# Performance work log

Measured on AMD Instinct MI355X. Metric: run time of the kernel, lower is better.

Reference implementation:

```python
import jax, jax.numpy as jnp
import numpy as np
from jax import lax
import math

B, CH, BINS, CROP = 8, 2, 1024, 1024
NUM_BANDS = 4
FF = 2048
EPS = 1e-5
SCALE = 0.02  # weight init scale for numeric stability


def _inorm(x, g, b):
    # InstanceNorm2d: x [B, C, H, W], normalize over (H, W) per (B, C); biased var
    m = x.mean(axis=(2, 3), keepdims=True)
    v = x.var(axis=(2, 3), keepdims=True)
    return (x - m) / jnp.sqrt(v + EPS) * g[None, :, None, None] + b[None, :, None, None]


def _dwconv(x, k):
    # depthwise conv1d: x [B, bins, W], k [bins, 1, 3], padding=1, groups=bins
    return lax.conv_general_dilated(x, k, (1,), [(1, 1)],
                                    dimension_numbers=('NCH', 'OIH', 'NCH'),
                                    feature_group_count=x.shape[1])


def setup_inputs() -> dict:
    key = jax.random.key(0)
    ks = jax.random.split(key, 12)
    inp = {
        'x': jax.random.normal(ks[0], (B, CH, BINS, CROP), jnp.float32),
        'prev_qk': jax.random.normal(ks[1], (B, NUM_BANDS, CROP, CROP), jnp.float32),
        'g_in': jnp.ones((CROP,), jnp.float32),
        'b_in': jnp.zeros((CROP,), jnp.float32),
        'W_in': jax.random.normal(ks[2], (1, CH), jnp.float32) * SCALE,
        'bias_in': jnp.zeros((1,), jnp.float32),
        'g1': jnp.ones((CROP,), jnp.float32),
        'b1': jnp.zeros((CROP,), jnp.float32),
        'Wq': jax.random.normal(ks[3], (BINS, BINS), jnp.float32) * SCALE,
        'Wk': jax.random.normal(ks[4], (BINS, BINS), jnp.float32) * SCALE,
        'Wv': jax.random.normal(ks[5], (BINS, BINS), jnp.float32) * SCALE,
        'Wo': jax.random.normal(ks[6], (BINS, BINS), jnp.float32) * SCALE,
        'kq': jax.random.normal(ks[7], (BINS, 1, 3), jnp.float32) * SCALE,
        'kk': jax.random.normal(ks[8], (BINS, 1, 3), jnp.float32) * SCALE,
        'kv': jax.random.normal(ks[9], (BINS, 1, 3), jnp.float32) * SCALE,
        'pos_w': jax.random.normal(ks[10], (BINS // NUM_BANDS, CROP), jnp.float32) * SCALE,
        'g2': jnp.ones((CROP,), jnp.float32),
        'b2': jnp.zeros((CROP,), jnp.float32),
        'W_ff': jax.random.normal(ks[11], (1, 2), jnp.float32) * SCALE,
        'bias_ff': jnp.zeros((1,), jnp.float32),
        'W1': jax.random.normal(jax.random.fold_in(key, 100), (FF, BINS), jnp.float32) * SCALE,
        'W2': jax.random.normal(jax.random.fold_in(key, 101), (BINS, FF), jnp.float32) * SCALE,
    }
    return inp


def reference(x, prev_qk, g_in, b_in, W_in, bias_in, g1, b1, Wq, Wk, Wv, Wo,
              kq, kk, kv, pos_w, g2, b2, W_ff, bias_ff, W1, W2):
    b = x.shape[0]
    nb = NUM_BANDS
    hd = BINS // nb
    # in_norm + in_project: transposed layout [B, CROP, BINS, CH]
    xt = jnp.transpose(x, (0, 3, 2, 1))
    xt = _inorm(xt, g_in, b_in)
    xt = jnp.einsum('bwhc,oc->bwho', xt, W_in) + bias_in  # [B,CROP,BINS,1]
    x0 = jnp.transpose(xt, (0, 3, 2, 1))                  # [B,1,BINS,CROP]
    # norm1 + attention over frames (w == CROP, c == BINS)
    h = jnp.transpose(_inorm(jnp.transpose(x0, (0, 3, 2, 1)), g1, b1), (0, 3, 2, 1))
    a_in = jnp.transpose(h, (0, 3, 2, 1))[..., 0]         # [B, W, BINS]
    q = jnp.einsum('bwc,oc->bwo', a_in, Wq)
    q = jnp.transpose(_dwconv(jnp.transpose(q, (0, 2, 1)), kq), (0, 2, 1))
    k = jnp.einsum('bwc,oc->bwo', a_in, Wk)
    k = jnp.transpose(_dwconv(jnp.transpose(k, (0, 2, 1)), kk), (0, 2, 1))
    v = jnp.einsum('bwc,oc->bwo', a_in, Wv)
    v = jnp.transpose(_dwconv(jnp.transpose(v, (0, 2, 1)), kv), (0, 2, 1))
    q4 = jnp.transpose(q.reshape(b, CROP, nb, hd), (0, 2, 1, 3))   # [B,nb,W,hd]
    k4 = jnp.transpose(k.reshape(b, CROP, nb, hd), (0, 2, 3, 1))   # [B,nb,hd,W]
    v4 = jnp.transpose(v.reshape(b, CROP, nb, hd), (0, 2, 1, 3))   # [B,nb,W,hd]
    # relative-position bias via pad-and-shift
    p = jnp.matmul(q4, pos_w)                                      # [B,nb,W,CROP]
    p = jnp.pad(p, ((0, 0), (0, 0), (0, 0), (1, 0)))
    p = jnp.swapaxes(p, 2, 3)[:, :, 1:, :]                         # [B,nb,CROP,W]
    qk = (jnp.matmul(q4, k4) + p) / math.sqrt(BINS)
    qk = qk + prev_qk
    a = jax.nn.softmax(qk, axis=-1)
    o = jnp.transpose(jnp.matmul(a, v4), (0, 2, 1, 3)).reshape(b, CROP, BINS)
    o = jnp.einsum('bwc,oc->bwo', o, Wo)                           # [B,W,BINS]
    h4 = jnp.transpose(o[..., None], (0, 3, 2, 1))                 # [B,1,BINS,CROP]
    x1 = jnp.concatenate([x0, h4], axis=1)                         # [B,2,BINS,CROP]
    # norm2 + ff_project + squared-ReLU FFN
    hn = _inorm(jnp.transpose(x1, (0, 3, 2, 1)), g2, b2)           # [B,CROP,BINS,2]
    hn = jnp.einsum('bwhc,oc->bwho', hn, W_ff) + bias_ff           # [B,CROP,BINS,1]
    hn = jnp.transpose(hn, (0, 3, 2, 1))                           # [B,1,BINS,CROP]
    ht = jnp.swapaxes(hn, 2, 3)                                    # [B,1,CROP,BINS]
    ht = jnp.square(jax.nn.relu(jnp.einsum('bowc,fc->bowf', ht, W1)))
    ht = jnp.einsum('bowf,cf->bowc', ht, W2)
    hf = jnp.swapaxes(ht, 2, 3)                                    # [B,1,BINS,CROP]
    out = jnp.concatenate([x1, hf], axis=1)                        # [B,3,BINS,CROP]
    return out, qk
```

## Files before the change

### kernel.cpp

```cpp
#include <hip/hip_runtime.h>
#include <stdint.h>

#define DEVI __device__ __forceinline__

typedef __attribute__((ext_vector_type(8))) short bf16x8;
typedef __attribute__((ext_vector_type(4))) float f32x4;

#define B_    8
#define CROP_ 1024
#define BINS_ 1024
#define NB_   4
#define HD_   256
#define FF_   2048
#define EPSF  1e-5f
#define OUT0_ELEMS (8ull*3ull*1024ull*1024ull)
#define MBYTE (1024ull*1024ull)
#define M1ELEM (1024ll*1024ll)
#define SMCAP 8.0f

DEVI unsigned short f2bf(float f) {
  unsigned u = __builtin_bit_cast(unsigned, f);
  u += 0x7fffu + ((u >> 16) & 1u);
  return (unsigned short)(u >> 16);
}
DEVI float bf2f(unsigned short h) {
  unsigned u = ((unsigned)h) << 16;
  return __builtin_bit_cast(float, u);
}

DEVI void gload16(const unsigned short* g, unsigned short* l) {
  __builtin_amdgcn_global_load_lds(
      (const __attribute__((address_space(1))) unsigned int*)g,
      (__attribute__((address_space(3))) unsigned int*)l, 16, 0, 0);
}

DEVI void xcdswz(int& bx, int& by, int& bz) {
  int gx = gridDim.x, gy = gridDim.y;
  int nwg = gx*gy*gridDim.z;
  int flat = blockIdx.x + gx*(blockIdx.y + gy*blockIdx.z);
  int s = (flat & 7)*(nwg >> 3) + (flat >> 3);
  bx = s % gx; s /= gx;
  by = s % gy;
  bz = s / gy;
}

__global__ __launch_bounds__(256) void k_conv_all(
    const float* __restrict__ Wq, const float* __restrict__ Wk,
    const float* __restrict__ Wv, const float* __restrict__ Wo,
    const float* __restrict__ W1, const float* __restrict__ W2,
    const float* __restrict__ pw,
    unsigned short* __restrict__ WQKVB, unsigned short* __restrict__ WOB,
    unsigned short* __restrict__ W1B, unsigned short* __restrict__ W2B,
    unsigned short* __restrict__ PWT) {
  long long i = (long long)blockIdx.x*256 + threadIdx.x;
  long long stride = (long long)gridDim.x*256;
  const long long total = 8*M1ELEM + (1 << 18);
  for (; i < total; i += stride) {
    if (i < 3*M1ELEM) {
      const float* s = i < M1ELEM ? Wq : (i < 2*M1ELEM ? Wk : Wv);
      WQKVB[i] = f2bf(s[i & (M1ELEM-1)]);
    } else if (i < 4*M1ELEM) { WOB[i-3*M1ELEM] = f2bf(Wo[i-3*M1ELEM]); }
    else if (i < 6*M1ELEM)   { W1B[i-4*M1ELEM] = f2bf(W1[i-4*M1ELEM]); }
    else if (i < 8*M1ELEM)   { W2B[i-6*M1ELEM] = f2bf(W2[i-6*M1ELEM]); }
    else {
      long long j = i - 8*M1ELEM;
      int w = (int)(j >> 8), d = (int)(j & 255);
      PWT[j] = f2bf(pw[d*1024 + w]);
    }
  }
}

__global__ __launch_bounds__(256) void k_instx0(const float* __restrict__ x,
    const float* __restrict__ g_in, const float* __restrict__ b_in,
    const float* __restrict__ W_in, const float* __restrict__ bias_in,
    float* __restrict__ outp, float* __restrict__ x0t) {
  int b = blockIdx.y, w0 = blockIdx.x*32;
  int t = threadIdx.x, wl = t & 31, p = t >> 5;
  const float* xb = x + (size_t)b*2*M1ELEM + w0 + wl;
  float s = 0.f, ss = 0.f;
  for (int i = p*256; i < p*256 + 256; ++i) {
    float v = xb[(size_t)i*CROP_];
    s += v; ss += v*v;
  }
  __shared__ float ls[8][32], lss[8][32];
  __shared__ float s_coef[32], s_add[32];
  ls[p][wl] = s; lss[p][wl] = ss;
  __syncthreads();
  float W0 = W_in[0], W1 = W_in[1], bi = bias_in[0];
  float sW = W0 + W1;
  if (t < 32) {
    float S = 0.f, SS = 0.f;
    for (int q = 0; q < 8; ++q) { S += ls[q][t]; SS += lss[q][t]; }
    float m = S*(1.f/2048.f);
    float var = SS*(1.f/2048.f) - m*m;
    float r = rsqrtf(var + EPSF);
    int w = w0 + t;
    float coef = r*g_in[w];
    s_coef[t] = coef;
    s_add[t] = b_in[w]*sW + bi - coef*m*sW;
  }
  __syncthreads();
  __shared__ float tile[32][33];
  int tx = wl, ty = p;
  float coef = s_coef[tx], add = s_add[tx];
  int w = w0 + tx;
  for (int h0 = 0; h0 < BINS_; h0 += 32) {
#pragma unroll
    for (int q = 0; q < 4; ++q) {
      int h = h0 + ty + q*8;
      size_t i0 = ((size_t)b*2*BINS_ + h)*CROP_ + w;
      float val = coef*(W0*x[i0] + W1*x[i0 + (size_t)M1ELEM]) + add;
      outp[(((size_t)b*3)*BINS_ + h)*CROP_ + w] = val;
      tile[ty + q*8][tx] = val;
    }
    __syncthreads();
#pragma unroll
    for (int q = 0; q < 4; ++q)
      x0t[((size_t)b*CROP_ + w0 + ty + q*8)*BINS_ + h0 + tx] = tile[tx][ty + q*8];
    __syncthreads();
  }
}

__global__ __launch_bounds__(256) void k_norm1(const float* __restrict__ x0t,
    const float* __restrict__ g1, const float* __restrict__ b1,
    unsigned short* __restrict__ ain) {
  int r = blockIdx.x;
  int w = r & (CROP_ - 1);
  int t = threadIdx.x;
  const float* row = x0t + (size_t)r*BINS_;
  float v[4], s = 0.f, ss = 0.f;
  for (int q = 0; q < 4; ++q) { v[q] = row[t + q*256]; s += v[q]; ss += v[q]*v[q]; }
  for (int off = 32; off; off >>= 1) { s += __shfl_xor(s, off); ss += __shfl_xor(ss, off); }
  __shared__ float red[8];
  int wv = t >> 6;
  if ((t & 63) == 0) { red[wv] = s; red[4 + wv] = ss; }
  __syncthreads();
  s = red[0] + red[1] + red[2] + red[3];
  ss = red[4] + red[5] + red[6] + red[7];
  float m = s*(1.f/1024.f);
  float var = ss*(1.f/1024.f) - m*m;
  float rs = rsqrtf(var + EPSF);
  float g = g1[w], bb = b1[w];
  for (int q = 0; q < 4; ++q)
    ain[(size_t)r*BINS_ + t + q*256] = f2bf((v[q] - m)*rs*g + bb);
}

__global__ __launch_bounds__(256) void k_norm2(const float* __restrict__ x0t,
    const float* __restrict__ o2,
    const float* __restrict__ g2, const float* __restrict__ b2,
    const float* __restrict__ W_ff, const float* __restrict__ bias_ff,
    unsigned short* __restrict__ hn) {
  int r = blockIdx.x;
  int w = r & (CROP_ - 1);
  int t = threadIdx.x;
  const float* ra = x0t + (size_t)r*BINS_;
  const float* rb = o2 + (size_t)r*BINS_;
  float va[4], vb[4], s = 0.f, ss = 0.f;
  for (int q = 0; q < 4; ++q) {
    va[q] = ra[t + q*256]; vb[q] = rb[t + q*256];
    s += va[q] + vb[q]; ss += va[q]*va[q] + vb[q]*vb[q];
  }
  for (int off = 32; off; off >>= 1) { s += __shfl_xor(s, off); ss += __shfl_xor(ss, off); }
  __shared__ float red[8];
  int wv = t >> 6;
  if ((t & 63) == 0) { red[wv] = s; red[4 + wv] = ss; }
  __syncthreads();
  s = red[0] + red[1] + red[2] + red[3];
  ss = red[4] + red[5] + red[6] + red[7];
  float m = s*(1.f/2048.f);
  float var = ss*(1.f/2048.f) - m*m;
  float rs = rsqrtf(var + EPSF);
  float W0 = W_ff[0], W1f = W_ff[1];
  float gg = g2[w]*rs;
  float add = b2[w]*(W0 + W1f) + bias_ff[0];
  for (int q = 0; q < 4; ++q)
    hn[(size_t)r*BINS_ + t + q*256] = f2bf(gg*(W0*(va[q] - m) + W1f*(vb[q] - m)) + add);
}

__global__ __launch_bounds__(256) void k_dwconv(const unsigned short* __restrict__ qkvb,
    const float* __restrict__ kq, const float* __restrict__ kk2,
    unsigned short* __restrict__ qkvc) {
  int w = blockIdx.x, b = blockIdx.y, which = blockIdx.z;
  int t = threadIdx.x;
  const float* kw = which == 0 ? kq : kk2;
  const unsigned short* r0 = qkvb + (size_t)which*8*M1ELEM + ((size_t)b*CROP_ + w)*BINS_;
  unsigned short* d0 = qkvc + (size_t)which*8*M1ELEM + ((size_t)b*CROP_ + w)*BINS_;
  for (int q = 0; q < 4; ++q) {
    int c = t + q*256;
    float k0 = kw[c*3], k1 = kw[c*3 + 1], k2 = kw[c*3 + 2];
    float acc = bf2f(r0[c]) * k1;
    if (w > 0)        acc += bf2f(r0[c - BINS_]) * k0;
    if (w < CROP_-1)  acc += bf2f(r0[c + BINS_]) * k2;
    d0[c] = f2bf(acc);
  }
}

__global__ __launch_bounds__(256) void k_dwconv_trV(const unsigned short* __restrict__ vb,
    const float* __restrict__ kv, unsigned short* __restrict__ vct) {
  int b = blockIdx.z;
  int w0 = blockIdx.x*32, c0 = blockIdx.y*32;
  int tx = threadIdx.x, ty = threadIdx.y;
  __shared__ unsigned short tile[34][33];
  const unsigned short* S = vb + (size_t)b*M1ELEM;
#pragma unroll
  for (int q = 0; q < 4; ++q) {
    int wl = ty + q*8;
    tile[wl + 1][tx] = S[(size_t)(w0 + wl)*BINS_ + c0 + tx];
  }
  if (ty == 0) tile[0][tx]  = (w0 > 0)          ? S[(size_t)(w0 - 1)*BINS_ + c0 + tx] : (unsigned short)0;
  if (ty == 1) tile[33][tx] = (w0 + 32 < CROP_) ? S[(size_t)(w0 + 32)*BINS_ + c0 + tx] : (unsigned short)0;
  __syncthreads();
  unsigned short* D = vct + (size_t)b*M1ELEM;
#pragma unroll
  for (int q = 0; q < 4; ++q) {
    int cl = ty + q*8;
    int c = c0 + cl;
    float k0 = kv[c*3], k1 = kv[c*3 + 1], k2 = kv[c*3 + 2];
    float val = k0*bf2f(tile[tx][cl]) + k1*bf2f(tile[tx + 1][cl]) + k2*bf2f(tile[tx + 2][cl]);
    D[(size_t)c*CROP_ + w0 + tx] = f2bf(val);
  }
}

#define BUFB 49152

template<int AC, int BC, int ABY>
DEVI void stage_gen(const unsigned short* Ab, int lda, const unsigned short* Bb, int ldb,
                    int k0, unsigned short* buf, int t, int wv) {
  int trow = t >> 3;
  int colel = ((t & 7) ^ (trow & 7)) << 3;
  unsigned short* lbase = buf + wv*512;
  const unsigned short* ga = Ab + (size_t)trow*lda + k0 + colel;
#pragma unroll
  for (int c = 0; c < AC; ++c)
    gload16(ga + (size_t)(c*64)*lda, lbase + c*4096);
  const unsigned short* gb = Bb + (size_t)trow*ldb + k0 + colel;
  unsigned short* lbb = buf + ABY/2 + wv*512;
#pragma unroll
  for (int c = 0; c < BC; ++c)
    gload16(gb + (size_t)(c*64)*ldb, lbb + c*4096);
}

#define RING_BODY(BOFF, ...)                                                           \
    bf16x8 af[2][4], bf[2][4];                                                         \
    _Pragma("unroll")                                                                  \
    for (int mi = 0; mi < 4; ++mi) {                                                   \
      int row = wm*64 + mi*16 + lr;                                                    \
      af[0][mi] = *(const bf16x8*)(bufc + ((row*128 + lk*16) ^ sx));                   \
    }                                                                                  \
    _Pragma("unroll")                                                                  \
    for (int ni = 0; ni < 4; ++ni) {                                                   \
      int row = wn*64 + ni*16 + lr;                                                    \
      bf[0][ni] = *(const bf16x8*)(bufc + BOFF + ((row*128 + lk*16) ^ sx));            \
    }                                                                                  \
    __builtin_amdgcn_sched_barrier(0);                                                 \
    _Pragma("unroll")                                                                  \
    for (int mi = 0; mi < 4; ++mi) {                                                   \
      int row = wm*64 + mi*16 + lr;                                                    \
      af[1][mi] = *(const bf16x8*)(bufc + ((row*128 + 64 + lk*16) ^ sx));              \
    }                                                                                  \
    _Pragma("unroll")                                                                  \
    for (int ni = 0; ni < 4; ++ni) {                                                   \
      int row = wn*64 + ni*16 + lr;                                                    \
      bf[1][ni] = *(const bf16x8*)(bufc + BOFF + ((row*128 + 64 + lk*16) ^ sx));       \
    }                                                                                  \
    asm volatile("s_waitcnt lgkmcnt(8)" ::: "memory");                                 \
    __builtin_amdgcn_sched_barrier(0);                                                 \
    __builtin_amdgcn_s_setprio(1);                                                     \
    _Pragma("unroll")                                                                  \
    for (int mi = 0; mi < 4; ++mi)                                                     \
      _Pragma("unroll")                                                                \
      for (int ni = 0; ni < 4; ++ni)                                                   \
        acc[mi][ni] = __builtin_amdgcn_mfma_f32_16x16x32_bf16(af[0][mi], bf[0][ni], acc[mi][ni], 0, 0, 0); \
    __builtin_amdgcn_s_setprio(0);                                                     \
    __builtin_amdgcn_sched_barrier(0);                                                 \
    asm volatile("s_waitcnt lgkmcnt(0)" ::: "memory");                                 \
    __builtin_amdgcn_s_barrier();                                                      \
    __VA_ARGS__;                                                                       \
    __builtin_amdgcn_s_setprio(1);                                                     \
    _Pragma("unroll")                                                                  \
    for (int mi = 0; mi < 4; ++mi)                                                     \
      _Pragma("unroll")                                                                \
      for (int ni = 0; ni < 4; ++ni)                                                   \
        acc[mi][ni] = __builtin_amdgcn_mfma_f32_16x16x32_bf16(af[1][mi], bf[1][ni], acc[mi][ni], 0, 0, 0); \
    __builtin_amdgcn_s_setprio(0);                                                     \
    if (kt + 1 < NT) {                                                                 \
      int rem = (NT-1 < kt+3 ? NT-1 : kt+3) - (kt+1);                                  \
      if (rem >= 2)      asm volatile("s_waitcnt vmcnt(12)" ::: "memory");             \
      else if (rem == 1) asm volatile("s_waitcnt vmcnt(6)"  ::: "memory");             \
      else               asm volatile("s_waitcnt vmcnt(0)"  ::: "memory");             \
      __builtin_amdgcn_s_barrier();                                                    \
    }

template<int MODE>
__global__ __launch_bounds__(512) void k_gemm3(
    const unsigned short* __restrict__ A, int lda,
    const unsigned short* __restrict__ Bt, int ldb,
    void* __restrict__ C, int ldc, int K, float* __restrict__ C2, int ch)
{
  __shared__ __align__(16) unsigned short lds[3*24576];
  int bxs, bys, bzs;
  xcdswz(bxs, bys, bzs);
  (void)bzs;
  const unsigned short* Ab = A + (size_t)bxs*256*lda;
  const unsigned short* Bb = Bt + (size_t)bys*128*ldb;
  const int t = threadIdx.x;
  const int wv = t >> 6, ln = t & 63;
  const int wm = wv >> 1, wn = wv & 1;
  const int lr = ln & 15, lk = ln >> 4;
  const int sx = (lr & 7) << 4;
  const int NT = K >> 6;
  stage_gen<4,2,32768>(Ab, lda, Bb, ldb, 0,   lds,           t, wv);
  stage_gen<4,2,32768>(Ab, lda, Bb, ldb, 64,  lds + 24576,   t, wv);
  stage_gen<4,2,32768>(Ab, lda, Bb, ldb, 128, lds + 49152,   t, wv);
  asm volatile("s_waitcnt vmcnt(12)" ::: "memory");
  __builtin_amdgcn_s_barrier();

  f32x4 acc[4][4] = {};
  for (int kt = 0; kt < NT; ++kt) {
    const int cur = kt % 3;
    const char* bufc = (const char*)lds + cur*BUFB;
    RING_BODY(32768,
      if (kt + 3 < NT) stage_gen<4,2,32768>(Ab, lda, Bb, ldb, (kt+3)*64,
                                            (unsigned short*)((char*)lds + cur*BUFB), t, wv))
  }

  if (MODE != 3) {
    const int row0 = bxs*256 + wm*64 + lk*4;
    const int col0 = bys*128 + wn*64 + lr;
#pragma unroll
    for (int mi = 0; mi < 4; ++mi)
#pragma unroll
      for (int ni = 0; ni < 4; ++ni)
#pragma unroll
        for (int j = 0; j < 4; ++j) {
          int row = row0 + mi*16 + j;
          int col = col0 + ni*16;
          float v = acc[mi][ni][j];
          if (MODE == 0 || MODE == 4) {
            ((float*)C)[(size_t)row*ldc + col] = v;
          } else if (MODE == 2) {
            float rr = fmaxf(v, 0.f);
            ((unsigned short*)C)[(size_t)row*ldc + col] = f2bf(rr*rr);
          } else if (MODE == 5) {
            ((unsigned short*)C)[(size_t)(col >> 10)*8*M1ELEM + (size_t)row*1024 + (col & 1023)] = f2bf(v);
          }
        }
  }
  if (MODE == 3 || MODE == 4) {
    __syncthreads();
    float* ldsT = (float*)lds + wv*4160;
#pragma unroll
    for (int mi = 0; mi < 4; ++mi)
#pragma unroll
      for (int ni = 0; ni < 4; ++ni)
#pragma unroll
        for (int j = 0; j < 4; ++j)
          ldsT[(ni*16 + lr)*65 + mi*16 + lk*4 + j] = acc[mi][ni][j];
    asm volatile("s_waitcnt lgkmcnt(0)" ::: "memory");
    int l16 = ln & 15, csub = ln >> 4;
    int b = bxs >> 2;
    int wbase = ((bxs & 3) << 8) + wm*64 + l16*4;
    float* outc = C2 + (((size_t)b*3 + ch)*BINS_)*CROP_;
#pragma unroll
    for (int cb = 0; cb < 16; ++cb) {
      int cl = cb*4 + csub;
      float4 v4;
      v4.x = ldsT[cl*65 + l16*4 + 0];
      v4.y = ldsT[cl*65 + l16*4 + 1];
      v4.z = ldsT[cl*65 + l16*4 + 2];
      v4.w = ldsT[cl*65 + l16*4 + 3];
      *(float4*)&outc[(size_t)(bys*128 + wn*64 + cl)*CROP_ + wbase] = v4;
    }
  }
}

DEVI void stage_qk(const unsigned short* qc_b, const unsigned short* kc_b,
                   const unsigned short* pwt, int bx, int by, int k0,
                   unsigned short* buf, int t, int wv) {
  int trow = t >> 3;
  int colel = ((t & 7) ^ (trow & 7)) << 3;
  unsigned short* lbase = buf + wv*512;
  if (k0 < 256) {
    const unsigned short* ga = qc_b + (size_t)(bx*256 + trow)*BINS_ + k0 + colel;
#pragma unroll
    for (int c = 0; c < 4; ++c)
      gload16(ga + (size_t)(c*64)*BINS_, lbase + c*4096);
  } else {
    const unsigned short* ga = pwt + (size_t)(bx*256 + trow)*HD_ + (k0 - 256) + colel;
#pragma unroll
    for (int c = 0; c < 4; ++c)
      gload16(ga + (size_t)(c*64)*HD_, lbase + c*4096);
  }
  const unsigned short* gbsrc = (k0 < 256) ? kc_b : qc_b;
  int kb = (k0 < 256) ? k0 : k0 - 256;
  const unsigned short* gb = gbsrc + (size_t)(by*128 + trow)*BINS_ + kb + colel;
  unsigned short* lbb = buf + 16384 + wv*512;
#pragma unroll
  for (int c = 0; c < 2; ++c)
    gload16(gb + (size_t)(c*64)*BINS_, lbb + c*4096);
}

__global__ __launch_bounds__(512) void k_qkpos2(
    const unsigned short* __restrict__ qc, const unsigned short* __restrict__ kc,
    const unsigned short* __restrict__ pwt,
    const float* __restrict__ prev, float* __restrict__ qkout,
    unsigned short* __restrict__ Pbuf, float* __restrict__ Lg)
{
  __shared__ __align__(16) unsigned short lds[3*24576];
  int bx, by, z;
  xcdswz(bx, by, z);
  const int b = z >> 2, n = z & 3;
  const size_t bandoff = (size_t)b*CROP_*BINS_ + (size_t)n*HD_;
  const unsigned short* qc_b = qc + bandoff;
  const unsigned short* kc_b = kc + bandoff;
  const int t = threadIdx.x;
  const int wv = t >> 6, ln = t & 63;
  const int wm = wv >> 1, wn = wv & 1;
  const int lr = ln & 15, lk = ln >> 4;
  const int sx = (lr & 7) << 4;
  const int NT = 8;
  stage_qk(qc_b, kc_b, pwt, bx, by, 0,   lds,         t, wv);
  stage_qk(qc_b, kc_b, pwt, bx, by, 64,  lds + 24576, t, wv);
  stage_qk(qc_b, kc_b, pwt, bx, by, 128, lds + 49152, t, wv);
  asm volatile("s_waitcnt vmcnt(12)" ::: "memory");
  __builtin_amdgcn_s_barrier();

  f32x4 acc[4][4] = {};
  for (int kt = 0; kt < NT; ++kt) {
    const int cur = kt % 3;
    const char* bufc = (const char*)lds + cur*BUFB;
    RING_BODY(32768,
      if (kt + 3 < NT) stage_qk(qc_b, kc_b, pwt, bx, by, (kt+3)*64,
                                (unsigned short*)((char*)lds + cur*BUFB), t, wv))
  }

  const float* pz = prev + (size_t)z*M1ELEM;
  float* oz = qkout + (size_t)z*M1ELEM;
  unsigned short* Pz = Pbuf + (size_t)z*M1ELEM;
  const int row0g = bx*256;
  const int col0 = by*128 + wn*64 + lr;
  float* slf = (float*)lds;
  const int rbase = wm*64 + lk*4;
#pragma unroll
  for (int mi = 0; mi < 4; ++mi) {
    float psum[4] = {0.f, 0.f, 0.f, 0.f};
#pragma unroll
    for (int ni = 0; ni < 4; ++ni)
#pragma unroll
      for (int j = 0; j < 4; ++j) {
        size_t idx = (size_t)(row0g + rbase + mi*16 + j)*CROP_ + col0 + ni*16;
        float val = acc[mi][ni][j]*0.03125f + pz[idx];
        oz[idx] = val;
        float p = __expf(val - SMCAP);
        Pz[idx] = f2bf(p);
        psum[j] += p;
      }
#pragma unroll
    for (int off = 1; off < 16; off <<= 1)
#pragma unroll
      for (int j = 0; j < 4; ++j) psum[j] += __shfl_xor(psum[j], off);
    if (lr == 0)
#pragma unroll
      for (int j = 0; j < 4; ++j) slf[wn*256 + rbase + mi*16 + j] = psum[j];
  }
  __syncthreads();
  if (t < 256) {
    size_t si = ((size_t)z*CROP_ + row0g + t)*8 + by;
    Lg[si] = slf[t] + slf[256 + t];
  }
}

__global__ __launch_bounds__(512) void k_pv3(
    const unsigned short* __restrict__ P, const float* __restrict__ Lg,
    const unsigned short* __restrict__ vct, unsigned short* __restrict__ ob)
{
  __shared__ __align__(16) unsigned short lds[3*24576];
  __shared__ float s_il[128];
  int bx, z, zz;
  xcdswz(bx, z, zz);
  (void)zz;
  const int b = z >> 2, band = z & 3;
  const unsigned short* Ab = P + (size_t)z*M1ELEM + (size_t)bx*128*CROP_;
  const unsigned short* Bb = vct + ((size_t)b*CROP_ + band*HD_)*CROP_;
  const int t = threadIdx.x;
  const int wv = t >> 6, ln = t & 63;
  const int wm = wv >> 2, wn = wv & 3;
  const int lr = ln & 15, lk = ln >> 4;
  const int sx = (lr & 7) << 4;
  const int NT = 16;
  if (t < 128) {
    size_t rg = (size_t)z*CROP_ + bx*128 + t;
    float l = 0.f;
#pragma unroll
    for (int cb = 0; cb < 8; ++cb) l += Lg[rg*8 + cb];
    s_il[t] = 1.f / l;
  }
  stage_gen<2,4,16384>(Ab, CROP_, Bb, CROP_, 0,   lds,         t, wv);
  stage_gen<2,4,16384>(Ab, CROP_, Bb, CROP_, 64,  lds + 24576, t, wv);
  stage_gen<2,4,16384>(Ab, CROP_, Bb, CROP_, 128, lds + 49152, t, wv);
  asm volatile("s_waitcnt vmcnt(12) lgkmcnt(0)" ::: "memory");
  __builtin_amdgcn_s_barrier();

  f32x4 acc[4][4] = {};
  for (int kt = 0; kt < NT; ++kt) {
    const int cur = kt % 3;
    const char* bufc = (const char*)lds + cur*BUFB;
    RING_BODY(16384,
      if (kt + 3 < NT) stage_gen<2,4,16384>(Ab, CROP_, Bb, CROP_, (kt+3)*64,
                                            (unsigned short*)((char*)lds + cur*BUFB), t, wv))
  }
#pragma unroll
  for (int mi = 0; mi < 4; ++mi)
#pragma unroll
    for (int j = 0; j < 4; ++j) {
      int rl = wm*64 + mi*16 + lk*4 + j;
      float il = s_il[rl];
#pragma unroll
      for (int ni = 0; ni < 4; ++ni) {
        int col = band*HD_ + wn*64 + ni*16 + lr;
        ob[((size_t)b*CROP_ + bx*128 + rl)*BINS_ + col] = f2bf(acc[mi][ni][j]*il);
      }
    }
}

extern "C" void kernel_launch(void* const* d_in, const int* in_sizes, int n_in,
                              void* d_out, int out_size, void* d_ws, size_t ws_size,
                              hipStream_t stream) {
  (void)in_sizes; (void)n_in; (void)out_size; (void)ws_size;
  const float* x       = (const float*)d_in[0];
  const float* prev_qk = (const float*)d_in[1];
  const float* g_in    = (const float*)d_in[2];
  const float* b_in    = (const float*)d_in[3];
  const float* W_in    = (const float*)d_in[4];
  const float* bias_in = (const float*)d_in[5];
  const float* g1      = (const float*)d_in[6];
  const float* b1      = (const float*)d_in[7];
  const float* Wq      = (const float*)d_in[8];
  const float* Wk      = (const float*)d_in[9];
  const float* Wv      = (const float*)d_in[10];
  const float* Wo      = (const float*)d_in[11];
  const float* kq      = (const float*)d_in[12];
  const float* kk      = (const float*)d_in[13];
  const float* kv      = (const float*)d_in[14];
  const float* pos_w   = (const float*)d_in[15];
  const float* g2      = (const float*)d_in[16];
  const float* b2      = (const float*)d_in[17];
  const float* W_ff    = (const float*)d_in[18];
  const float* bias_ff = (const float*)d_in[19];
  const float* W1      = (const float*)d_in[20];
  const float* W2      = (const float*)d_in[21];

  char* ws = (char*)d_ws;
  unsigned short* WQKVB = (unsigned short*)(ws + 0*MBYTE);
  unsigned short* WOB   = (unsigned short*)(ws + 6*MBYTE);
  unsigned short* W1B   = (unsigned short*)(ws + 8*MBYTE);
  unsigned short* W2B   = (unsigned short*)(ws + 12*MBYTE);
  unsigned short* PWT   = (unsigned short*)(ws + 16*MBYTE);
  float*          Lg    = (float*)(ws + 17*MBYTE);
  float*          X0T   = (float*)(ws + 20*MBYTE);
  unsigned short* AIN   = (unsigned short*)(ws + 52*MBYTE);
  unsigned short* QKVB  = (unsigned short*)(ws + 68*MBYTE);
  unsigned short* PBUF  = (unsigned short*)(ws + 52*MBYTE);
  unsigned short* QKVC  = (unsigned short*)(ws + 116*MBYTE);
  float*          O2    = (float*)(ws + 116*MBYTE);
  unsigned short* OB    = (unsigned short*)(ws + 148*MBYTE);
  unsigned short* VCT   = (unsigned short*)(ws + 164*MBYTE);
  unsigned short* HN    = (unsigned short*)(ws + 52*MBYTE);
  unsigned short* HT    = (unsigned short*)(ws + 20*MBYTE);

  float* outp  = (float*)d_out;
  float* qkout = outp + OUT0_ELEMS;

  dim3 blk256(256, 1, 1);
  dim3 blk512(512, 1, 1);
  dim3 blk32x8(32, 8, 1);

  k_conv_all<<<8448, blk256, 0, stream>>>(Wq, Wk, Wv, Wo, W1, W2, pos_w,
                                          WQKVB, WOB, W1B, W2B, PWT);
  k_instx0<<<dim3(32, 8, 1), blk256, 0, stream>>>(x, g_in, b_in, W_in, bias_in, outp, X0T);
  k_norm1<<<8192, blk256, 0, stream>>>(X0T, g1, b1, AIN);
  k_gemm3<5><<<dim3(32, 24, 1), blk512, 0, stream>>>(AIN, 1024, WQKVB, 1024, QKVB, 0, 1024, nullptr, 0);
  k_dwconv<<<dim3(1024, 8, 2), blk256, 0, stream>>>(QKVB, kq, kk, QKVC);
  k_dwconv_trV<<<dim3(32, 32, 8), blk32x8, 0, stream>>>(QKVB + (size_t)2*8*M1ELEM, kv, VCT);
  k_qkpos2<<<dim3(4, 8, 32), blk512, 0, stream>>>(QKVC, QKVC + (size_t)8*M1ELEM, PWT,
                                                  prev_qk, qkout, PBUF, Lg);
  k_pv3<<<dim3(8, 32, 1), blk512, 0, stream>>>(PBUF, Lg, VCT, OB);
  k_gemm3<4><<<dim3(32, 8, 1), blk512, 0, stream>>>(OB, 1024, WOB, 1024, O2, 1024, 1024, outp, 1);
  k_norm2<<<8192, blk256, 0, stream>>>(X0T, O2, g2, b2, W_ff, bias_ff, HN);
  k_gemm3<2><<<dim3(32, 16, 1), blk512, 0, stream>>>(HN, 1024, W1B, 1024, HT, 2048, 1024, nullptr, 0);
  k_gemm3<3><<<dim3(32, 8, 1), blk512, 0, stream>>>(HT, 2048, W2B, 2048, nullptr, 1024, 2048, outp, 2);
}
```

Baseline: 469.0 us.

## Fuse norm1 into instx0, vectorize dwconv, drop XCD swizzle, simplify MFMA ring

Folds the norm1 pass into k_instx0 by accumulating per-column statistics while writing x0, then re-reading the rows just written to emit the bf16 normalized input. This removes one kernel launch and a separate stats pass. The depthwise conv now processes four channels per thread with vector loads. The XCD block swizzle is removed from the GEMM, QK and PV kernels, and the MFMA ring body no longer splits LDS loads and compute into two interleaved halves. Dropping the swizzle and the interleave may hurt L2 locality and latency hiding, and the fused kernel runs on only 256 blocks, so the norm work has limited parallelism.

Measured after the change: 450.9 us. -3.9%, faster.

```diff
diff --git a/kernel.cpp b/kernel.cpp
--- a/kernel.cpp
+++ b/kernel.cpp
@@ -32,16 +32,6 @@
   __builtin_amdgcn_global_load_lds(
       (const __attribute__((address_space(1))) unsigned int*)g,
       (__attribute__((address_space(3))) unsigned int*)l, 16, 0, 0);
-}
-
-DEVI void xcdswz(int& bx, int& by, int& bz) {
-  int gx = gridDim.x, gy = gridDim.y;
-  int nwg = gx*gy*gridDim.z;
-  int flat = blockIdx.x + gx*(blockIdx.y + gy*blockIdx.z);
-  int s = (flat & 7)*(nwg >> 3) + (flat >> 3);
-  bx = s % gx; s /= gx;
-  by = s % gy;
-  bz = s / gy;
 }
 
 __global__ __launch_bounds__(256) void k_conv_all(
@@ -73,7 +63,9 @@
 __global__ __launch_bounds__(256) void k_instx0(const float* __restrict__ x,
     const float* __restrict__ g_in, const float* __restrict__ b_in,
     const float* __restrict__ W_in, const float* __restrict__ bias_in,
-    float* __restrict__ outp, float* __restrict__ x0t) {
+    const float* __restrict__ g1, const float* __restrict__ b1,
+    float* __restrict__ outp, float* __restrict__ x0t,
+    unsigned short* __restrict__ ain) {
   int b = blockIdx.y, w0 = blockIdx.x*32;
   int t = threadIdx.x, wl = t & 31, p = t >> 5;
   const float* xb = x + (size_t)b*2*M1ELEM + w0 + wl;
@@ -84,6 +76,7 @@
   }
   __shared__ float ls[8][32], lss[8][32];
   __shared__ float s_coef[32], s_add[32];
+  __shared__ float s_cm[32], s_ca[32];
   ls[p][wl] = s; lss[p][wl] = ss;
   __syncthreads();
   float W0 = W_in[0], W1 = W_in[1], bi = bias_in[0];
@@ -104,6 +97,7 @@
   int tx = wl, ty = p;
   float coef = s_coef[tx], add = s_add[tx];
   int w = w0 + tx;
+  float s1 = 0.f, ss1 = 0.f;
   for (int h0 = 0; h0 < BINS_; h0 += 32) {
 #pragma unroll
     for (int q = 0; q < 4; ++q) {
@@ -112,6 +106,7 @@
       float val = coef*(W0*x[i0] + W1*x[i0 + (size_t)M1ELEM]) + add;
       outp[(((size_t)b*3)*BINS_ + h)*CROP_ + w] = val;
       tile[ty + q*8][tx] = val;
+      s1 += val; ss1 += val*val;
     }
     __syncthreads();
 #pragma unroll
@@ -119,30 +114,31 @@
       x0t[((size_t)b*CROP_ + w0 + ty + q*8)*BINS_ + h0 + tx] = tile[tx][ty + q*8];
     __syncthreads();
   }
-}
-
-__global__ __launch_bounds__(256) void k_norm1(const float* __restrict__ x0t,
-    const float* __restrict__ g1, const float* __restrict__ b1,
-    unsigned short* __restrict__ ain) {
-  int r = blockIdx.x;
-  int w = r & (CROP_ - 1);
-  int t = threadIdx.x;
-  const float* row = x0t + (size_t)r*BINS_;
-  float v[4], s = 0.f, ss = 0.f;
-  for (int q = 0; q < 4; ++q) { v[q] = row[t + q*256]; s += v[q]; ss += v[q]*v[q]; }
-  for (int off = 32; off; off >>= 1) { s += __shfl_xor(s, off); ss += __shfl_xor(ss, off); }
-  __shared__ float red[8];
-  int wv = t >> 6;
-  if ((t & 63) == 0) { red[wv] = s; red[4 + wv] = ss; }
-  __syncthreads();
-  s = red[0] + red[1] + red[2] + red[3];
-  ss = red[4] + red[5] + red[6] + red[7];
-  float m = s*(1.f/1024.f);
-  float var = ss*(1.f/1024.f) - m*m;
-  float rs = rsqrtf(var + EPSF);
-  float g = g1[w], bb = b1[w];
-  for (int q = 0; q < 4; ++q)
-    ain[(size_t)r*BINS_ + t + q*256] = f2bf((v[q] - m)*rs*g + bb);
+  ls[p][wl] = s1; lss[p][wl] = ss1;
+  __syncthreads();
+  if (t < 32) {
+    float S = 0.f, SS = 0.f;
+    for (int q = 0; q < 8; ++q) { S += ls[q][t]; SS += lss[q][t]; }
+    float m = S*(1.f/1024.f);
+    float var = SS*(1.f/1024.f) - m*m;
+    float rs = rsqrtf(var + EPSF);
+    int ww = w0 + t;
+    float cm = rs*g1[ww];
+    s_cm[t] = cm;
+    s_ca[t] = b1[ww] - m*cm;
+  }
+  __syncthreads();
+  for (int wloc = 0; wloc < 32; ++wloc) {
+    float cm = s_cm[wloc], ca = s_ca[wloc];
+    const float* row = x0t + ((size_t)b*CROP_ + w0 + wloc)*BINS_;
+    float4 v = *(const float4*)&row[t*4];
+    ushort4 o;
+    o.x = f2bf(v.x*cm + ca);
+    o.y = f2bf(v.y*cm + ca);
+    o.z = f2bf(v.z*cm + ca);
+    o.w = f2bf(v.w*cm + ca);
+    *(ushort4*)&ain[((size_t)b*CROP_ + w0 + wloc)*BINS_ + t*4] = o;
+  }
 }
 
 __global__ __launch_bounds__(256) void k_norm2(const float* __restrict__ x0t,
@@ -185,14 +181,26 @@
   const float* kw = which == 0 ? kq : kk2;
   const unsigned short* r0 = qkvb + (size_t)which*8*M1ELEM + ((size_t)b*CROP_ + w)*BINS_;
   unsigned short* d0 = qkvc + (size_t)which*8*M1ELEM + ((size_t)b*CROP_ + w)*BINS_;
-  for (int q = 0; q < 4; ++q) {
-    int c = t + q*256;
-    float k0 = kw[c*3], k1 = kw[c*3 + 1], k2 = kw[c*3 + 2];
-    float acc = bf2f(r0[c]) * k1;
-    if (w > 0)        acc += bf2f(r0[c - BINS_]) * k0;
-    if (w < CROP_-1)  acc += bf2f(r0[c + BINS_]) * k2;
-    d0[c] = f2bf(acc);
-  }
+  int c4 = t*4;
+  float kf[12];
+  *(float4*)&kf[0] = *(const float4*)&kw[c4*3];
+  *(float4*)&kf[4] = *(const float4*)&kw[c4*3 + 4];
+  *(float4*)&kf[8] = *(const float4*)&kw[c4*3 + 8];
+  ushort4 vm = *(const ushort4*)&r0[c4];
+  ushort4 va = make_ushort4(0,0,0,0), vbn = make_ushort4(0,0,0,0);
+  if (w > 0)        va  = *(const ushort4*)&r0[c4 - BINS_];
+  if (w < CROP_-1)  vbn = *(const ushort4*)&r0[c4 + BINS_];
+  const unsigned short* vmp = (const unsigned short*)&vm;
+  const unsigned short* vap = (const unsigned short*)&va;
+  const unsigned short* vbp = (const unsigned short*)&vbn;
+  ushort4 o;
+  unsigned short* op = (unsigned short*)&o;
+#pragma unroll
+  for (int j = 0; j < 4; ++j) {
+    float acc = bf2f(vmp[j])*kf[3*j + 1] + bf2f(vap[j])*kf[3*j] + bf2f(vbp[j])*kf[3*j + 2];
+    op[j] = f2bf(acc);
+  }
+  *(ushort4*)&d0[c4] = o;
 }
 
 __global__ __launch_bounds__(256) void k_dwconv_trV(const unsigned short* __restrict__ vb,
@@ -243,45 +251,29 @@
 #define RING_BODY(BOFF, ...)                                                           \
     bf16x8 af[2][4], bf[2][4];                                                         \
     _Pragma("unroll")                                                                  \
-    for (int mi = 0; mi < 4; ++mi) {                                                   \
-      int row = wm*64 + mi*16 + lr;                                                    \
-      af[0][mi] = *(const bf16x8*)(bufc + ((row*128 + lk*16) ^ sx));                   \
+    for (int kk = 0; kk < 2; ++kk) {                                                   \
+      _Pragma("unroll")                                                                \
+      for (int mi = 0; mi < 4; ++mi) {                                                 \
+        int row = wm*64 + mi*16 + lr;                                                  \
+        af[kk][mi] = *(const bf16x8*)(bufc + ((row*128 + kk*64 + lk*16) ^ sx));        \
+      }                                                                                \
+      _Pragma("unroll")                                                                \
+      for (int ni = 0; ni < 4; ++ni) {                                                 \
+        int row = wn*64 + ni*16 + lr;                                                  \
+        bf[kk][ni] = *(const bf16x8*)(bufc + BOFF + ((row*128 + kk*64 + lk*16) ^ sx)); \
+      }                                                                                \
     }                                                                                  \
-    _Pragma("unroll")                                                                  \
-    for (int ni = 0; ni < 4; ++ni) {                                                   \
-      int row = wn*64 + ni*16 + lr;                                                    \
-      bf[0][ni] = *(const bf16x8*)(bufc + BOFF + ((row*128 + lk*16) ^ sx));            \
-    }                                                                                  \
-    __builtin_amdgcn_sched_barrier(0);                                                 \
-    _Pragma("unroll")                                                                  \
-    for (int mi = 0; mi < 4; ++mi) {                                                   \
-      int row = wm*64 + mi*16 + lr;                                                    \
-      af[1][mi] = *(const bf16x8*)(bufc + ((row*128 + 64 + lk*16) ^ sx));              \
-    }                                                                                  \
-    _Pragma("unroll")                                                                  \
-    for (int ni = 0; ni < 4; ++ni) {                                                   \
-      int row = wn*64 + ni*16 + lr;                                                    \
-      bf[1][ni] = *(const bf16x8*)(bufc + BOFF + ((row*128 + 64 + lk*16) ^ sx));       \
-    }                                                                                  \
-    asm volatile("s_waitcnt lgkmcnt(8)" ::: "memory");                                 \
-    __builtin_amdgcn_sched_barrier(0);                                                 \
-    __builtin_amdgcn_s_setprio(1);                                                     \
-    _Pragma("unroll")                                                                  \
-    for (int mi = 0; mi < 4; ++mi)                                                     \
-      _Pragma("unroll")                                                                \
-      for (int ni = 0; ni < 4; ++ni)                                                   \
-        acc[mi][ni] = __builtin_amdgcn_mfma_f32_16x16x32_bf16(af[0][mi], bf[0][ni], acc[mi][ni], 0, 0, 0); \
-    __builtin_amdgcn_s_setprio(0);                                                     \
-    __builtin_amdgcn_sched_barrier(0);                                                 \
     asm volatile("s_waitcnt lgkmcnt(0)" ::: "memory");                                 \
     __builtin_amdgcn_s_barrier();                                                      \
     __VA_ARGS__;                                                                       \
     __builtin_amdgcn_s_setprio(1);                                                     \
     _Pragma("unroll")                                                                  \
-    for (int mi = 0; mi < 4; ++mi)                                                     \
+    for (int kk = 0; kk < 2; ++kk)                                                     \
       _Pragma("unroll")                                                                \
-      for (int ni = 0; ni < 4; ++ni)                                                   \
-        acc[mi][ni] = __builtin_amdgcn_mfma_f32_16x16x32_bf16(af[1][mi], bf[1][ni], acc[mi][ni], 0, 0, 0); \
+      for (int mi = 0; mi < 4; ++mi)                                                   \
+        _Pragma("unroll")                                                              \
+        for (int ni = 0; ni < 4; ++ni)                                                 \
+          acc[mi][ni] = __builtin_amdgcn_mfma_f32_16x16x32_bf16(af[kk][mi], bf[kk][ni], acc[mi][ni], 0, 0, 0); \
     __builtin_amdgcn_s_setprio(0);                                                     \
     if (kt + 1 < NT) {                                                                 \
       int rem = (NT-1 < kt+3 ? NT-1 : kt+3) - (kt+1);                                  \
@@ -298,11 +290,8 @@
     void* __restrict__ C, int ldc, int K, float* __restrict__ C2, int ch)
 {
   __shared__ __align__(16) unsigned short lds[3*24576];
-  int bxs, bys, bzs;
-  xcdswz(bxs, bys, bzs);
-  (void)bzs;
-  const unsigned short* Ab = A + (size_t)bxs*256*lda;
-  const unsigned short* Bb = Bt + (size_t)bys*128*ldb;
+  const unsigned short* Ab = A + (size_t)blockIdx.x*256*lda;
+  const unsigned short* Bb = Bt + (size_t)blockIdx.y*128*ldb;
   const int t = threadIdx.x;
   const int wv = t >> 6, ln = t & 63;
   const int wm = wv >> 1, wn = wv & 1;
@@ -325,8 +314,8 @@
   }
 
   if (MODE != 3) {
-    const int row0 = bxs*256 + wm*64 + lk*4;
-    const int col0 = bys*128 + wn*64 + lr;
+    const int row0 = blockIdx.x*256 + wm*64 + lk*4;
+    const int col0 = blockIdx.y*128 + wn*64 + lr;
 #pragma unroll
     for (int mi = 0; mi < 4; ++mi)
 #pragma unroll
@@ -358,8 +347,8 @@
           ldsT[(ni*16 + lr)*65 + mi*16 + lk*4 + j] = acc[mi][ni][j];
     asm volatile("s_waitcnt lgkmcnt(0)" ::: "memory");
     int l16 = ln & 15, csub = ln >> 4;
-    int b = bxs >> 2;
-    int wbase = ((bxs & 3) << 8) + wm*64 + l16*4;
+    int b = blockIdx.x >> 2;
+    int wbase = ((blockIdx.x & 3) << 8) + wm*64 + l16*4;
     float* outc = C2 + (((size_t)b*3 + ch)*BINS_)*CROP_;
 #pragma unroll
     for (int cb = 0; cb < 16; ++cb) {
@@ -369,7 +358,7 @@
       v4.y = ldsT[cl*65 + l16*4 + 1];
       v4.z = ldsT[cl*65 + l16*4 + 2];
       v4.w = ldsT[cl*65 + l16*4 + 3];
-      *(float4*)&outc[(size_t)(bys*128 + wn*64 + cl)*CROP_ + wbase] = v4;
+      *(float4*)&outc[(size_t)(blockIdx.y*128 + wn*64 + cl)*CROP_ + wbase] = v4;
     }
   }
 }
@@ -407,12 +396,11 @@
     unsigned short* __restrict__ Pbuf, float* __restrict__ Lg)
 {
   __shared__ __align__(16) unsigned short lds[3*24576];
-  int bx, by, z;
-  xcdswz(bx, by, z);
-  const int b = z >> 2, n = z & 3;
+  const int z = blockIdx.z, b = z >> 2, n = z & 3;
   const size_t bandoff = (size_t)b*CROP_*BINS_ + (size_t)n*HD_;
   const unsigned short* qc_b = qc + bandoff;
   const unsigned short* kc_b = kc + bandoff;
+  const int bx = blockIdx.x, by = blockIdx.y;
   const int t = threadIdx.x;
   const int wv = t >> 6, ln = t & 63;
   const int wm = wv >> 1, wn = wv & 1;
@@ -476,10 +464,8 @@
 {
   __shared__ __align__(16) unsigned short lds[3*24576];
   __shared__ float s_il[128];
-  int bx, z, zz;
-  xcdswz(bx, z, zz);
-  (void)zz;
-  const int b = z >> 2, band = z & 3;
+  const int z = blockIdx.y, b = z >> 2, band = z & 3;
+  const int bx = blockIdx.x;
   const unsigned short* Ab = P + (size_t)z*M1ELEM + (size_t)bx*128*CROP_;
   const unsigned short* Bb = vct + ((size_t)b*CROP_ + band*HD_)*CROP_;
   const int t = threadIdx.x;
@@ -577,8 +563,8 @@
 
   k_conv_all<<<8448, blk256, 0, stream>>>(Wq, Wk, Wv, Wo, W1, W2, pos_w,
                                           WQKVB, WOB, W1B, W2B, PWT);
-  k_instx0<<<dim3(32, 8, 1), blk256, 0, stream>>>(x, g_in, b_in, W_in, bias_in, outp, X0T);
-  k_norm1<<<8192, blk256, 0, stream>>>(X0T, g1, b1, AIN);
+  k_instx0<<<dim3(32, 8, 1), blk256, 0, stream>>>(x, g_in, b_in, W_in, bias_in,
+                                                  g1, b1, outp, X0T, AIN);
   k_gemm3<5><<<dim3(32, 24, 1), blk512, 0, stream>>>(AIN, 1024, WQKVB, 1024, QKVB, 0, 1024, nullptr, 0);
   k_dwconv<<<dim3(1024, 8, 2), blk256, 0, stream>>>(QKVB, kq, kk, QKVC);
   k_dwconv_trV<<<dim3(32, 32, 8), blk32x8, 0, stream>>>(QKVB + (size_t)2*8*M1ELEM, kv, VCT);
```
